# Optimization experiments

Measured on AMD Instinct MI355X. Metric: run time of the kernel, lower is better.

Reference implementation:

```python
import jax, jax.numpy as jnp
import numpy as np

B, S, D, H = 2, 2048, 1024, 16
HD = D // H


def setup_inputs() -> dict:
    key = jax.random.key(0)
    ks = jax.random.split(key, 9)
    sc = 0.02
    return {
        "x": jax.random.normal(ks[0], (B, S, D), dtype=jnp.float32),
        "qw": jax.random.normal(ks[1], (D, D), dtype=jnp.float32) * sc,
        "qb": jax.random.normal(ks[2], (D,), dtype=jnp.float32) * sc,
        "kw": jax.random.normal(ks[3], (D, D), dtype=jnp.float32) * sc,
        "kb": jax.random.normal(ks[4], (D,), dtype=jnp.float32) * sc,
        "vw": jax.random.normal(ks[5], (D, D), dtype=jnp.float32) * sc,
        "vb": jax.random.normal(ks[6], (D,), dtype=jnp.float32) * sc,
        "ow": jax.random.normal(ks[7], (D, D), dtype=jnp.float32) * sc,
        "ob": jax.random.normal(ks[8], (D,), dtype=jnp.float32) * sc,
    }


def reference(x, qw, qb, kw, kb, vw, vb, ow, ob):
    b, s, d = x.shape
    # projections (torch Linear: x @ W.T + b)
    q = (x @ qw.T + qb).reshape(b, s, H, HD).transpose(0, 2, 1, 3)  # bhsd
    k = (x @ kw.T + kb).reshape(b, s, H, HD).transpose(0, 2, 1, 3)
    v = (x @ vw.T + vb).reshape(b, s, H, HD).transpose(0, 2, 1, 3)
    scale = 1.0 / jnp.sqrt(jnp.float32(HD))
    score = jnp.einsum("bhsd,bhtd->bhst", q, k) * scale  # bhss
    # causal mask: -inf strictly above diagonal
    mask = jnp.triu(jnp.full((s, s), -jnp.inf, dtype=score.dtype), k=1)
    score = jax.nn.softmax(score + mask, axis=-1)
    o = jnp.einsum("bhst,bhtd->bhsd", score, v)
    o = o.transpose(0, 2, 1, 3).reshape(b, s, d)
    return o @ ow.T + ob
```

## Files before the change

kernel.cpp:

```cpp
#include <hip/hip_runtime.h>
#include <hip/hip_bf16.h>
#include <stdint.h>

typedef __bf16 bf16x8 __attribute__((ext_vector_type(8)));
typedef float f32x4 __attribute__((ext_vector_type(4)));
typedef unsigned short ushort_t;


__device__ inline ushort_t f2bf(float f) {
  union { float f; uint32_t u; } v; v.f = f;
  uint32_t r = (v.u + 0x7fffu + ((v.u >> 16) & 1u)) >> 16;
  return (ushort_t)r;
}

__device__ inline void gll16(const void* g, void* l) {
  __builtin_amdgcn_global_load_lds((const __attribute__((address_space(1))) void*)g,
                                   (__attribute__((address_space(3))) void*)l, 16, 0, 0);
}

__global__ void cvt_x(const float* __restrict__ in, ushort_t* __restrict__ out) {
  int i = blockIdx.x * blockDim.x + threadIdx.x;
  float4 f = ((const float4*)in)[i];
  union { ushort_t u[4]; uint2 v; } r;
  r.u[0] = f2bf(f.x); r.u[1] = f2bf(f.y); r.u[2] = f2bf(f.z); r.u[3] = f2bf(f.w);
  ((uint2*)out)[i] = r.v;
}
__global__ void cvt_w(const float* __restrict__ a, const float* __restrict__ b,
                      const float* __restrict__ c, const float* __restrict__ d,
                      ushort_t* __restrict__ out) {
  const float* srcs[4] = {a, b, c, d};
  const float* s = srcs[blockIdx.y];
  ushort_t* o = out + (size_t)blockIdx.y * 1048576;
  int i = blockIdx.x * blockDim.x + threadIdx.x;
  float4 f = ((const float4*)s)[i];
  union { ushort_t u[4]; uint2 v; } r;
  r.u[0] = f2bf(f.x); r.u[1] = f2bf(f.y); r.u[2] = f2bf(f.z); r.u[3] = f2bf(f.w);
  ((uint2*)(o))[i] = r.v;
}

__global__ __launch_bounds__(256) void qkv_gemm(
    const ushort_t* __restrict__ xb,
    const ushort_t* __restrict__ qwb, const ushort_t* __restrict__ kwb, const ushort_t* __restrict__ vwb,
    const float* __restrict__ qbias, const float* __restrict__ kbias, const float* __restrict__ vbias,
    ushort_t* __restrict__ qo, ushort_t* __restrict__ ko, ushort_t* __restrict__ vto)
{
  const int z = blockIdx.z;
  const ushort_t* W = (z == 0) ? qwb : (z == 1) ? kwb : vwb;
  const float* bias = (z == 0) ? qbias : (z == 1) ? kbias : vbias;

  __shared__ __align__(16) ushort_t As[128 * 32];
  __shared__ __align__(16) ushort_t Bs[128 * 32];

  const int tid = threadIdx.x;
  const int w = tid >> 6;
  const int lane = tid & 63;
  const int ln = lane & 15;
  const int q4 = lane >> 4;
  const int wm = w & 1, wn = w >> 1;
  const int m0 = blockIdx.y * 128;
  const int n0 = blockIdx.x * 128;

  f32x4 acc[4][4];
  #pragma unroll
  for (int i = 0; i < 4; i++)
    #pragma unroll
    for (int j = 0; j < 4; j++) acc[i][j] = f32x4{0.f, 0.f, 0.f, 0.f};

  for (int k0 = 0; k0 < 1024; k0 += 32) {
    __syncthreads();
    #pragma unroll
    for (int i = 0; i < 2; i++) {
      int c = tid + i * 256;
      int row = c >> 2, cq = c & 3;
      gll16(&xb[(size_t)(m0 + row) * 1024 + k0 + cq * 8], &As[c * 8]);
      gll16(&W [(size_t)(n0 + row) * 1024 + k0 + cq * 8], &Bs[c * 8]);
    }
    __syncthreads();
    bf16x8 af[4], bfr[4];
    #pragma unroll
    for (int t = 0; t < 4; t++) {
      af[t]  = *(const bf16x8*)(&As[(wm * 64 + t * 16 + ln) * 32 + q4 * 8]);
      bfr[t] = *(const bf16x8*)(&Bs[(wn * 64 + t * 16 + ln) * 32 + q4 * 8]);
    }
    #pragma unroll
    for (int tm = 0; tm < 4; tm++)
      #pragma unroll
      for (int tn = 0; tn < 4; tn++)
        acc[tm][tn] = __builtin_amdgcn_mfma_f32_16x16x32_bf16(af[tm], bfr[tn], acc[tm][tn], 0, 0, 0);
  }

  #pragma unroll
  for (int tn = 0; tn < 4; tn++) {
    int col = n0 + wn * 64 + tn * 16 + ln;
    float bv = bias[col];
    int h = col >> 6, hd = col & 63;
    #pragma unroll
    for (int tm = 0; tm < 4; tm++) {
      int rowb = m0 + wm * 64 + tm * 16 + q4 * 4;
      #pragma unroll
      for (int r = 0; r < 4; r++) {
        int row = rowb + r;
        int b = row >> 11, s = row & 2047;
        float val = acc[tm][tn][r] + bv;
        if (z == 0) {
          qo[((size_t)((b * 16 + h) * 2048 + s)) * 64 + hd] = f2bf(val * 0.180336884f);
        } else if (z == 1) {
          ko[((size_t)((b * 16 + h) * 2048 + s)) * 64 + hd] = f2bf(val);
        } else {
          vto[((size_t)((b * 16 + h) * 64 + hd)) * 2048 + s] = f2bf(val);
        }
      }
    }
  }
}

#define PAD 72
__global__ __launch_bounds__(256) void attn(
    const ushort_t* __restrict__ qp, const ushort_t* __restrict__ kp,
    const ushort_t* __restrict__ vtp, ushort_t* __restrict__ op)
{
  __shared__ __align__(16) ushort_t Ks[64 * PAD];
  __shared__ __align__(16) ushort_t Vts[64 * PAD];
  __shared__ __align__(16) ushort_t Ps[4][16 * PAD];

  const int tid = threadIdx.x;
  const int w = tid >> 6;
  const int lane = tid & 63;
  const int ln = lane & 15;
  const int q4 = lane >> 4;
  const int bh = blockIdx.y;
  const int b = bh >> 4, h = bh & 15;
  const int qt = (blockIdx.x + blockIdx.y) & 31;
  const int q0 = qt * 64;
  const int nt = qt + 1;

  const int c0 = tid, c1 = tid + 256;
  const int kr0_row = c0 >> 3, kr0_col = (c0 & 7) * 8;
  const int kr1_row = c1 >> 3, kr1_col = (c1 & 7) * 8;

  bf16x8 onesf;
  {
    union { ushort_t u[8]; bf16x8 v; } t;
    #pragma unroll
    for (int j = 0; j < 8; j++) t.u[j] = 0x3F80;
    onesf = t.v;
  }

  bf16x8 qf0, qf1;
  {
    const ushort_t* base = qp + ((size_t)bh * 2048 + q0 + w * 16 + ln) * 64 + q4 * 8;
    qf0 = *(const bf16x8*)(base);
    qf1 = *(const bf16x8*)(base + 32);
  }

  f32x4 acc_o[4];
  f32x4 acc_l = f32x4{0.f, 0.f, 0.f, 0.f};
  #pragma unroll
  for (int t = 0; t < 4; t++) acc_o[t] = f32x4{0.f, 0.f, 0.f, 0.f};

  uint4 kr0, kr1, vr0, vr1;
  {
    const ushort_t* kb = kp + (size_t)bh * 2048 * 64;
    kr0 = *(const uint4*)(kb + kr0_row * 64 + kr0_col);
    kr1 = *(const uint4*)(kb + kr1_row * 64 + kr1_col);
    const ushort_t* vb = vtp + (size_t)bh * 64 * 2048;
    vr0 = *(const uint4*)(vb + (size_t)kr0_row * 2048 + kr0_col);
    vr1 = *(const uint4*)(vb + (size_t)kr1_row * 2048 + kr1_col);
  }

  for (int it = 0; it < nt; it++) {
    if (it) __syncthreads();
    *(uint4*)(&Ks [kr0_row * PAD + kr0_col]) = kr0;
    *(uint4*)(&Ks [kr1_row * PAD + kr1_col]) = kr1;
    *(uint4*)(&Vts[kr0_row * PAD + kr0_col]) = vr0;
    *(uint4*)(&Vts[kr1_row * PAD + kr1_col]) = vr1;
    __syncthreads();

    if (it + 1 < nt) {
      int kv1 = (it + 1) * 64;
      const ushort_t* kb = kp + ((size_t)bh * 2048 + kv1) * 64;
      kr0 = *(const uint4*)(kb + kr0_row * 64 + kr0_col);
      kr1 = *(const uint4*)(kb + kr1_row * 64 + kr1_col);
      const ushort_t* vb = vtp + (size_t)bh * 64 * 2048;
      vr0 = *(const uint4*)(vb + (size_t)kr0_row * 2048 + kv1 + kr0_col);
      vr1 = *(const uint4*)(vb + (size_t)kr1_row * 2048 + kv1 + kr1_col);
    }

    f32x4 sc[4];
    #pragma unroll
    for (int t = 0; t < 4; t++) sc[t] = f32x4{0.f, 0.f, 0.f, 0.f};
    #pragma unroll
    for (int ks = 0; ks < 2; ks++) {
      bf16x8 qk = ks ? qf1 : qf0;
      #pragma unroll
      for (int tn = 0; tn < 4; tn++) {
        bf16x8 kf = *(const bf16x8*)(&Ks[(tn * 16 + ln) * PAD + ks * 32 + q4 * 8]);
        sc[tn] = __builtin_amdgcn_mfma_f32_16x16x32_bf16(qk, kf, sc[tn], 0, 0, 0);
      }
    }
    if (it == nt - 1) {
      int qrow = q0 + w * 16 + q4 * 4;
      int kv0 = it * 64;
      #pragma unroll
      for (int tn = 0; tn < 4; tn++) {
        int col = kv0 + tn * 16 + ln;
        #pragma unroll
        for (int r = 0; r < 4; r++)
          if (col > qrow + r) sc[tn][r] = -__builtin_inff();
      }
    }
    #pragma unroll
    for (int tn = 0; tn < 4; tn++)
      #pragma unroll
      for (int r = 0; r < 4; r++) {
        float p = __builtin_amdgcn_exp2f(sc[tn][r]);
        Ps[w][(q4 * 4 + r) * PAD + tn * 16 + ln] = (ushort_t)(__float_as_uint(p) >> 16);
      }
    #pragma unroll
    for (int ks = 0; ks < 2; ks++) {
      bf16x8 pf = *(const bf16x8*)(&Ps[w][ln * PAD + ks * 32 + q4 * 8]);
      acc_l = __builtin_amdgcn_mfma_f32_16x16x32_bf16(pf, onesf, acc_l, 0, 0, 0);
      #pragma unroll
      for (int tn = 0; tn < 4; tn++) {
        bf16x8 vf = *(const bf16x8*)(&Vts[(tn * 16 + ln) * PAD + ks * 32 + q4 * 8]);
        acc_o[tn] = __builtin_amdgcn_mfma_f32_16x16x32_bf16(pf, vf, acc_o[tn], 0, 0, 0);
      }
    }
  }

  float invl[4];
  #pragma unroll
  for (int r = 0; r < 4; r++) invl[r] = __builtin_amdgcn_rcpf(acc_l[r]);
  #pragma unroll
  for (int tn = 0; tn < 4; tn++)
    #pragma unroll
    for (int r = 0; r < 4; r++) {
      int row = q0 + w * 16 + q4 * 4 + r;
      op[((size_t)b * 2048 + row) * 1024 + h * 64 + tn * 16 + ln] = f2bf(acc_o[tn][r] * invl[r]);
    }
}

__global__ __launch_bounds__(256) void out_gemm(
    const ushort_t* __restrict__ ob_in, const ushort_t* __restrict__ owb,
    const float* __restrict__ obias, float* __restrict__ out)
{
  __shared__ __align__(16) ushort_t As[64 * 32];
  __shared__ __align__(16) ushort_t Bs[128 * 32];

  const int tid = threadIdx.x;
  const int w = tid >> 6;
  const int lane = tid & 63;
  const int ln = lane & 15;
  const int q4 = lane >> 4;
  const int wm = w & 1, wn = w >> 1;
  const int m0 = blockIdx.y * 64;
  const int n0 = blockIdx.x * 128;

  f32x4 acc[2][4];
  #pragma unroll
  for (int i = 0; i < 2; i++)
    #pragma unroll
    for (int j = 0; j < 4; j++) acc[i][j] = f32x4{0.f, 0.f, 0.f, 0.f};

  for (int k0 = 0; k0 < 1024; k0 += 32) {
    __syncthreads();
    {
      int rowA = tid >> 2, cqA = tid & 3;
      gll16(&ob_in[(size_t)(m0 + rowA) * 1024 + k0 + cqA * 8], &As[tid * 8]);
      gll16(&owb  [(size_t)(n0 + rowA) * 1024 + k0 + cqA * 8], &Bs[tid * 8]);
      int c2 = tid + 256;
      int rowB = c2 >> 2, cqB = c2 & 3;
      gll16(&owb  [(size_t)(n0 + rowB) * 1024 + k0 + cqB * 8], &Bs[c2 * 8]);
    }
    __syncthreads();
    bf16x8 af[2], bfr[4];
    #pragma unroll
    for (int t = 0; t < 2; t++)
      af[t] = *(const bf16x8*)(&As[(wm * 32 + t * 16 + ln) * 32 + q4 * 8]);
    #pragma unroll
    for (int t = 0; t < 4; t++)
      bfr[t] = *(const bf16x8*)(&Bs[(wn * 64 + t * 16 + ln) * 32 + q4 * 8]);
    #pragma unroll
    for (int tm = 0; tm < 2; tm++)
      #pragma unroll
      for (int tn = 0; tn < 4; tn++)
        acc[tm][tn] = __builtin_amdgcn_mfma_f32_16x16x32_bf16(af[tm], bfr[tn], acc[tm][tn], 0, 0, 0);
  }

  #pragma unroll
  for (int tn = 0; tn < 4; tn++) {
    int col = n0 + wn * 64 + tn * 16 + ln;
    float bv = obias[col];
    #pragma unroll
    for (int tm = 0; tm < 2; tm++) {
      int rowb = m0 + wm * 32 + tm * 16 + q4 * 4;
      #pragma unroll
      for (int r = 0; r < 4; r++)
        out[(size_t)(rowb + r) * 1024 + col] = acc[tm][tn][r] + bv;
    }
  }
}

extern "C" void kernel_launch(void* const* d_in, const int* in_sizes, int n_in,
                              void* d_out, int out_size, void* d_ws, size_t ws_size,
                              hipStream_t stream) {
  const float* x     = (const float*)d_in[0];
  const float* qw    = (const float*)d_in[1];
  const float* qb    = (const float*)d_in[2];
  const float* kw    = (const float*)d_in[3];
  const float* kb    = (const float*)d_in[4];
  const float* vw    = (const float*)d_in[5];
  const float* vb    = (const float*)d_in[6];
  const float* ow    = (const float*)d_in[7];
  const float* obias = (const float*)d_in[8];
  float* out = (float*)d_out;

  char* ws = (char*)d_ws;
  ushort_t* xb  = (ushort_t*)(ws);
  ushort_t* wb  = (ushort_t*)(ws + 8388608);
  ushort_t* qwb = wb;
  ushort_t* kwb = wb + 1048576;
  ushort_t* vwb = wb + 2097152;
  ushort_t* owb = wb + 3145728;
  ushort_t* qo  = (ushort_t*)(ws + 16777216);
  ushort_t* ko  = (ushort_t*)(ws + 25165824);
  ushort_t* vto = (ushort_t*)(ws + 33554432);
  ushort_t* oo  = (ushort_t*)(ws + 41943040);

  cvt_x<<<dim3(4096), dim3(256), 0, stream>>>(x, xb);
  cvt_w<<<dim3(1024, 4), dim3(256), 0, stream>>>(qw, kw, vw, ow, wb);

  qkv_gemm<<<dim3(8, 32, 3), dim3(256), 0, stream>>>(xb, qwb, kwb, vwb, qb, kb, vb, qo, ko, vto);
  attn<<<dim3(32, 32), dim3(256), 0, stream>>>(qo, ko, vto, oo);
  out_gemm<<<dim3(8, 64), dim3(256), 0, stream>>>(oo, owb, obias, out);
}
```

Baseline: 194.7 us.

## Double attention query tile per block and transpose V projection GEMM for coalesced stores

The attention kernel now processes 128 query rows per block, with each wave handling two 16-row slices. This reuses each loaded K/V tile and its fragments across twice as many queries, halving global K/V traffic and LDS fragment reads per query. Query tiles are assigned in mirrored order across the two halves of the grid so long and short causal tiles are mixed. For the V projection, the GEMM swaps its operands to compute V-transpose directly, so its stores run contiguous along the sequence. The change costs more registers per wave, which may reduce occupancy, and the grid has only half as many blocks.

```diff
diff --git a/kernel.cpp b/kernel.cpp
--- a/kernel.cpp
+++ b/kernel.cpp
@@ -45,8 +45,19 @@
     ushort_t* __restrict__ qo, ushort_t* __restrict__ ko, ushort_t* __restrict__ vto)
 {
   const int z = blockIdx.z;
-  const ushort_t* W = (z == 0) ? qwb : (z == 1) ? kwb : vwb;
   const float* bias = (z == 0) ? qbias : (z == 1) ? kbias : vbias;
+  const ushort_t* Ap;
+  const ushort_t* Bp;
+  int m0, n0;
+  if (z == 2) {
+    Ap = vwb; Bp = xb;
+    m0 = blockIdx.x * 128;
+    n0 = blockIdx.y * 128;
+  } else {
+    Ap = xb; Bp = (z == 0) ? qwb : kwb;
+    m0 = blockIdx.y * 128;
+    n0 = blockIdx.x * 128;
+  }
 
   __shared__ __align__(16) ushort_t As[128 * 32];
   __shared__ __align__(16) ushort_t Bs[128 * 32];
@@ -57,8 +68,6 @@
   const int ln = lane & 15;
   const int q4 = lane >> 4;
   const int wm = w & 1, wn = w >> 1;
-  const int m0 = blockIdx.y * 128;
-  const int n0 = blockIdx.x * 128;
 
   f32x4 acc[4][4];
   #pragma unroll
@@ -72,8 +81,8 @@
     for (int i = 0; i < 2; i++) {
       int c = tid + i * 256;
       int row = c >> 2, cq = c & 3;
-      gll16(&xb[(size_t)(m0 + row) * 1024 + k0 + cq * 8], &As[c * 8]);
-      gll16(&W [(size_t)(n0 + row) * 1024 + k0 + cq * 8], &Bs[c * 8]);
+      gll16(&Ap[(size_t)(m0 + row) * 1024 + k0 + cq * 8], &As[c * 8]);
+      gll16(&Bp[(size_t)(n0 + row) * 1024 + k0 + cq * 8], &Bs[c * 8]);
     }
     __syncthreads();
     bf16x8 af[4], bfr[4];
@@ -89,25 +98,41 @@
         acc[tm][tn] = __builtin_amdgcn_mfma_f32_16x16x32_bf16(af[tm], bfr[tn], acc[tm][tn], 0, 0, 0);
   }
 
-  #pragma unroll
-  for (int tn = 0; tn < 4; tn++) {
-    int col = n0 + wn * 64 + tn * 16 + ln;
-    float bv = bias[col];
-    int h = col >> 6, hd = col & 63;
-    #pragma unroll
-    for (int tm = 0; tm < 4; tm++) {
-      int rowb = m0 + wm * 64 + tm * 16 + q4 * 4;
-      #pragma unroll
-      for (int r = 0; r < 4; r++) {
-        int row = rowb + r;
-        int b = row >> 11, s = row & 2047;
-        float val = acc[tm][tn][r] + bv;
-        if (z == 0) {
-          qo[((size_t)((b * 16 + h) * 2048 + s)) * 64 + hd] = f2bf(val * 0.180336884f);
-        } else if (z == 1) {
-          ko[((size_t)((b * 16 + h) * 2048 + s)) * 64 + hd] = f2bf(val);
-        } else {
-          vto[((size_t)((b * 16 + h) * 64 + hd)) * 2048 + s] = f2bf(val);
+  if (z == 2) {
+    #pragma unroll
+    for (int tn = 0; tn < 4; tn++) {
+      int col = n0 + wn * 64 + tn * 16 + ln;
+      int bb = col >> 11, s = col & 2047;
+      size_t base = (size_t)bb * 2097152 + s;
+      #pragma unroll
+      for (int tm = 0; tm < 4; tm++) {
+        int prow = m0 + wm * 64 + tm * 16 + q4 * 4;
+        #pragma unroll
+        for (int r = 0; r < 4; r++) {
+          int p = prow + r;
+          vto[base + (size_t)p * 2048] = f2bf(acc[tm][tn][r] + bias[p]);
+        }
+      }
+    }
+  } else {
+    #pragma unroll
+    for (int tn = 0; tn < 4; tn++) {
+      int col = n0 + wn * 64 + tn * 16 + ln;
+      float bv = bias[col];
+      int h = col >> 6, hd = col & 63;
+      #pragma unroll
+      for (int tm = 0; tm < 4; tm++) {
+        int rowb = m0 + wm * 64 + tm * 16 + q4 * 4;
+        #pragma unroll
+        for (int r = 0; r < 4; r++) {
+          int row = rowb + r;
+          int b = row >> 11, s = row & 2047;
+          float val = acc[tm][tn][r] + bv;
+          if (z == 0) {
+            qo[((size_t)((b * 16 + h) * 2048 + s)) * 64 + hd] = f2bf(val * 0.180336884f);
+          } else {
+            ko[((size_t)((b * 16 + h) * 2048 + s)) * 64 + hd] = f2bf(val);
+          }
         }
       }
     }
@@ -121,7 +146,7 @@
 {
   __shared__ __align__(16) ushort_t Ks[64 * PAD];
   __shared__ __align__(16) ushort_t Vts[64 * PAD];
-  __shared__ __align__(16) ushort_t Ps[4][16 * PAD];
+  __shared__ __align__(16) ushort_t Ps[8][16 * PAD];
 
   const int tid = threadIdx.x;
   const int w = tid >> 6;
@@ -130,9 +155,10 @@
   const int q4 = lane >> 4;
   const int bh = blockIdx.y;
   const int b = bh >> 4, h = bh & 15;
-  const int qt = (blockIdx.x + blockIdx.y) & 31;
-  const int q0 = qt * 64;
-  const int nt = qt + 1;
+  int tswz = (blockIdx.x + blockIdx.y) & 15;
+  const int qt = (blockIdx.y & 16) ? (15 - tswz) : tswz;
+  const int q0 = qt * 128;
+  const int nt = 2 * qt + 2;
 
   const int c0 = tid, c1 = tid + 256;
   const int kr0_row = c0 >> 3, kr0_col = (c0 & 7) * 8;
@@ -146,17 +172,22 @@
     onesf = t.v;
   }
 
-  bf16x8 qf0, qf1;
-  {
-    const ushort_t* base = qp + ((size_t)bh * 2048 + q0 + w * 16 + ln) * 64 + q4 * 8;
-    qf0 = *(const bf16x8*)(base);
-    qf1 = *(const bf16x8*)(base + 32);
-  }
-
-  f32x4 acc_o[4];
-  f32x4 acc_l = f32x4{0.f, 0.f, 0.f, 0.f};
-  #pragma unroll
-  for (int t = 0; t < 4; t++) acc_o[t] = f32x4{0.f, 0.f, 0.f, 0.f};
+  bf16x8 qf[2][2];
+  #pragma unroll
+  for (int s = 0; s < 2; s++) {
+    const ushort_t* base = qp + ((size_t)bh * 2048 + q0 + w * 32 + s * 16 + ln) * 64 + q4 * 8;
+    qf[s][0] = *(const bf16x8*)(base);
+    qf[s][1] = *(const bf16x8*)(base + 32);
+  }
+
+  f32x4 acc_o[2][4];
+  f32x4 acc_l[2];
+  #pragma unroll
+  for (int s = 0; s < 2; s++) {
+    acc_l[s] = f32x4{0.f, 0.f, 0.f, 0.f};
+    #pragma unroll
+    for (int t = 0; t < 4; t++) acc_o[s][t] = f32x4{0.f, 0.f, 0.f, 0.f};
+  }
 
   uint4 kr0, kr1, vr0, vr1;
   {
@@ -186,58 +217,77 @@
       vr1 = *(const uint4*)(vb + (size_t)kr1_row * 2048 + kv1 + kr1_col);
     }
 
-    f32x4 sc[4];
-    #pragma unroll
-    for (int t = 0; t < 4; t++) sc[t] = f32x4{0.f, 0.f, 0.f, 0.f};
+    f32x4 sc[2][4];
+    #pragma unroll
+    for (int s = 0; s < 2; s++)
+      #pragma unroll
+      for (int t = 0; t < 4; t++) sc[s][t] = f32x4{0.f, 0.f, 0.f, 0.f};
     #pragma unroll
     for (int ks = 0; ks < 2; ks++) {
-      bf16x8 qk = ks ? qf1 : qf0;
-      #pragma unroll
-      for (int tn = 0; tn < 4; tn++) {
-        bf16x8 kf = *(const bf16x8*)(&Ks[(tn * 16 + ln) * PAD + ks * 32 + q4 * 8]);
-        sc[tn] = __builtin_amdgcn_mfma_f32_16x16x32_bf16(qk, kf, sc[tn], 0, 0, 0);
-      }
-    }
-    if (it == nt - 1) {
-      int qrow = q0 + w * 16 + q4 * 4;
+      bf16x8 kf[4];
+      #pragma unroll
+      for (int tn = 0; tn < 4; tn++)
+        kf[tn] = *(const bf16x8*)(&Ks[(tn * 16 + ln) * PAD + ks * 32 + q4 * 8]);
+      #pragma unroll
+      for (int s = 0; s < 2; s++)
+        #pragma unroll
+        for (int tn = 0; tn < 4; tn++)
+          sc[s][tn] = __builtin_amdgcn_mfma_f32_16x16x32_bf16(qf[s][ks], kf[tn], sc[s][tn], 0, 0, 0);
+    }
+    if (it >= 2 * qt) {
       int kv0 = it * 64;
       #pragma unroll
-      for (int tn = 0; tn < 4; tn++) {
-        int col = kv0 + tn * 16 + ln;
-        #pragma unroll
-        for (int r = 0; r < 4; r++)
-          if (col > qrow + r) sc[tn][r] = -__builtin_inff();
-      }
-    }
+      for (int s = 0; s < 2; s++) {
+        int qrow = q0 + w * 32 + s * 16 + q4 * 4;
+        #pragma unroll
+        for (int tn = 0; tn < 4; tn++) {
+          int col = kv0 + tn * 16 + ln;
+          #pragma unroll
+          for (int r = 0; r < 4; r++)
+            if (col > qrow + r) sc[s][tn][r] = -__builtin_inff();
+        }
+      }
+    }
+    #pragma unroll
+    for (int s = 0; s < 2; s++)
+      #pragma unroll
+      for (int tn = 0; tn < 4; tn++)
+        #pragma unroll
+        for (int r = 0; r < 4; r++) {
+          float p = __builtin_amdgcn_exp2f(sc[s][tn][r]);
+          Ps[w * 2 + s][(q4 * 4 + r) * PAD + tn * 16 + ln] = (ushort_t)(__float_as_uint(p) >> 16);
+        }
+    #pragma unroll
+    for (int ks = 0; ks < 2; ks++) {
+      bf16x8 vf[4];
+      #pragma unroll
+      for (int tn = 0; tn < 4; tn++)
+        vf[tn] = *(const bf16x8*)(&Vts[(tn * 16 + ln) * PAD + ks * 32 + q4 * 8]);
+      #pragma unroll
+      for (int s = 0; s < 2; s++) {
+        bf16x8 pf = *(const bf16x8*)(&Ps[w * 2 + s][ln * PAD + ks * 32 + q4 * 8]);
+        acc_l[s] = __builtin_amdgcn_mfma_f32_16x16x32_bf16(pf, onesf, acc_l[s], 0, 0, 0);
+        #pragma unroll
+        for (int tn = 0; tn < 4; tn++)
+          acc_o[s][tn] = __builtin_amdgcn_mfma_f32_16x16x32_bf16(pf, vf[tn], acc_o[s][tn], 0, 0, 0);
+      }
+    }
+  }
+
+  #pragma unroll
+  for (int s = 0; s < 2; s++) {
+    float invl[4];
+    #pragma unroll
+    for (int r = 0; r < 4; r++) invl[r] = __builtin_amdgcn_rcpf(acc_l[s][r]);
     #pragma unroll
     for (int tn = 0; tn < 4; tn++)
       #pragma unroll
       for (int r = 0; r < 4; r++) {
-        float p = __builtin_amdgcn_exp2f(sc[tn][r]);
-        Ps[w][(q4 * 4 + r) * PAD + tn * 16 + ln] = (ushort_t)(__float_as_uint(p) >> 16);
-      }
-    #pragma unroll
-    for (int ks = 0; ks < 2; ks++) {
-      bf16x8 pf = *(const bf16x8*)(&Ps[w][ln * PAD + ks * 32 + q4 * 8]);
-      acc_l = __builtin_amdgcn_mfma_f32_16x16x32_bf16(pf, onesf, acc_l, 0, 0, 0);
-      #pragma unroll
-      for (int tn = 0; tn < 4; tn++) {
-        bf16x8 vf = *(const bf16x8*)(&Vts[(tn * 16 + ln) * PAD + ks * 32 + q4 * 8]);
-        acc_o[tn] = __builtin_amdgcn_mfma_f32_16x16x32_bf16(pf, vf, acc_o[tn], 0, 0, 0);
-      }
-    }
-  }
-
-  float invl[4];
-  #pragma unroll
-  for (int r = 0; r < 4; r++) invl[r] = __builtin_amdgcn_rcpf(acc_l[r]);
-  #pragma unroll
-  for (int tn = 0; tn < 4; tn++)
-    #pragma unroll
-    for (int r = 0; r < 4; r++) {
-      int row = q0 + w * 16 + q4 * 4 + r;
-      op[((size_t)b * 2048 + row) * 1024 + h * 64 + tn * 16 + ln] = f2bf(acc_o[tn][r] * invl[r]);
-    }
+        int row = q0 + w * 32 + s * 16 + q4 * 4 + r;
+        op[((size_t)b * 2048 + row) * 1024 + h * 64 + tn * 16 + ln] =
+            f2bf(acc_o[s][tn][r] * invl[r]);
+      }
+  }
 }
 
 __global__ __launch_bounds__(256) void out_gemm(
@@ -331,6 +381,6 @@
   cvt_w<<<dim3(1024, 4), dim3(256), 0, stream>>>(qw, kw, vw, ow, wb);
 
   qkv_gemm<<<dim3(8, 32, 3), dim3(256), 0, stream>>>(xb, qwb, kwb, vwb, qb, kb, vb, qo, ko, vto);
-  attn<<<dim3(32, 32), dim3(256), 0, stream>>>(qo, ko, vto, oo);
+  attn<<<dim3(16, 32), dim3(256), 0, stream>>>(qo, ko, vto, oo);
   out_gemm<<<dim3(8, 64), dim3(256), 0, stream>>>(oo, owb, obias, out);
 }
```

After: 198.1 us. Within noise of the previous version (+1.8%).
